# Performance work log

Hardware: AMD Instinct MI355X
Metric: run time of the kernel (lower is better)

Reference implementation:

```python
import jax, jax.numpy as jnp
import numpy as np

EPS = 1e-06


def setup_inputs() -> dict:
    key = jax.random.key(0)
    k1, k2 = jax.random.split(key, 2)
    B, C, T = 8, 256, 8192
    x_real = jax.random.normal(k1, (B, C, T), dtype=jnp.float32)
    x_imag = jax.random.normal(k2, (B, C, T), dtype=jnp.float32)
    # elementwise_affine init: identity * 1/sqrt(2), zero bias
    eye = jnp.eye(2, dtype=jnp.float32)[:, :, None]  # (2,2,1)
    weight = jnp.broadcast_to(eye * 0.70710678118, (2, 2, C)).astype(jnp.float32)
    bias = jnp.zeros((2, C), dtype=jnp.float32)
    return {"x_real": x_real, "x_imag": x_imag, "weight": weight, "bias": bias}


def reference(x_real, x_imag, weight, bias):
    C = x_real.shape[1]
    # (B, C, T, 2) complex-as-last-axis layout
    x = jnp.stack([x_real, x_imag], axis=-1)
    mu = jnp.mean(x, axis=1, keepdims=True)          # per-(b,t) mean over channels
    xc = x - mu                                      # (B, C, T, 2)
    # 2x2 covariance per (b, t), + eps*I for numerical stability
    V = jnp.einsum('bcti,bctj->btij', xc, xc) / C
    V = V + EPS * jnp.eye(2, dtype=x.dtype)
    # Symmetric 2x2 eigendecomposition -> inverse-sqrt whitening matrix
    L, Q = jnp.linalg.eigh(V)                        # L: (B,T,2), Q: (B,T,2,2)
    W = jnp.einsum('btik,btk,btjk->btij', Q, L ** -0.5, Q)  # Q diag(L^-1/2) Q^T
    z = jnp.einsum('bcti,btij->bctj', xc, W)         # whitened (B,C,T,2)
    # per-channel 2x2 affine + bias
    y = jnp.einsum('bcti,ijc->bctj', z, weight) + bias.T[None, :, None, :]
    return y[..., 0], y[..., 1]
```

## Files before the change

### kernel.cpp

```cpp
#include <hip/hip_runtime.h>
#include <math.h>

#define EPS_CLN 1e-6f

constexpr int Bb = 8;
constexpr int Cc = 256;
constexpr int Tt = 8192;

constexpr int TT   = 32;
constexpr int CPT  = 8;
constexpr int NCG  = Cc / CPT;
constexpr int NT4  = TT / 4;
constexpr int NTHR = NCG * NT4;
constexpr int NTB  = Tt / TT;

__global__ __launch_bounds__(NTHR, 4)
void cln_kernel(const float* __restrict__ xr_g, const float* __restrict__ xi_g,
                const float* __restrict__ wgt, const float* __restrict__ bs,
                float* __restrict__ yr_g, float* __restrict__ yi_g) {
    __shared__ float red[5][NCG][TT];
    __shared__ float wlds[5][TT];

    const int tid = threadIdx.x;
    const int t4i = tid & (NT4 - 1);
    const int cg  = tid >> 3;
    const int tb  = blockIdx.x & (NTB - 1);
    const int b   = blockIdx.x >> 8;
    const int tl  = t4i * 4;

    const int cbase = cg * CPT;
    const int base  = (b * Cc + cbase) * Tt + tb * TT + tl;

    float4 xr[CPT], xi[CPT];
#pragma unroll
    for (int k = 0; k < CPT; ++k) {
        xr[k] = *(const float4*)(xr_g + base + k * Tt);
        xi[k] = *(const float4*)(xi_g + base + k * Tt);
    }

    float4 sr = make_float4(0.f, 0.f, 0.f, 0.f);
    float4 si = sr, srr = sr, sri = sr, sii = sr;
#pragma unroll
    for (int k = 0; k < CPT; ++k) {
#define ACC1(c) { float r = xr[k].c, m = xi[k].c;          \
        sr.c += r; si.c += m;                              \
        srr.c = fmaf(r, r, srr.c);                         \
        sri.c = fmaf(r, m, sri.c);                         \
        sii.c = fmaf(m, m, sii.c); }
        ACC1(x) ACC1(y) ACC1(z) ACC1(w)
#undef ACC1
    }

    *(float4*)&red[0][cg][tl] = sr;
    *(float4*)&red[1][cg][tl] = si;
    *(float4*)&red[2][cg][tl] = srr;
    *(float4*)&red[3][cg][tl] = sri;
    *(float4*)&red[4][cg][tl] = sii;
    __syncthreads();

    if (tid < 5 * TT) {
        const int st = tid >> 5;
        const int t  = tid & (TT - 1);
        float s = 0.f;
#pragma unroll
        for (int g = 0; g < NCG; ++g) s += red[st][g][t];
        wlds[st][t] = s;
    }
    __syncthreads();

    if (tid < TT) {
        const float invC = 1.0f / (float)Cc;
        const float mur = wlds[0][tid] * invC, mui = wlds[1][tid] * invC;
        const float a  = fmaf(-mur, mur, wlds[2][tid] * invC) + EPS_CLN;
        const float bb = fmaf(-mur, mui, wlds[3][tid] * invC);
        const float d  = fmaf(-mui, mui, wlds[4][tid] * invC) + EPS_CLN;
        const float s   = sqrtf(fmaf(-bb, bb, a * d));
        const float tau = sqrtf(a + d + 2.0f * s);
        const float inv = 1.0f / (s * tau);
        wlds[0][tid] = mur;
        wlds[1][tid] = mui;
        wlds[2][tid] = (d + s) * inv;
        wlds[3][tid] = -bb * inv;
        wlds[4][tid] = (a + s) * inv;
    }
    __syncthreads();

    const float4 mur = *(const float4*)&wlds[0][tl];
    const float4 mui = *(const float4*)&wlds[1][tl];
    const float4 w00 = *(const float4*)&wlds[2][tl];
    const float4 w01 = *(const float4*)&wlds[3][tl];
    const float4 w11 = *(const float4*)&wlds[4][tl];

#pragma unroll
    for (int k = 0; k < CPT; ++k) {
        const int c = cbase + k;
        const float wt00 = wgt[c];
        const float wt01 = wgt[Cc + c];
        const float wt10 = wgt[2 * Cc + c];
        const float wt11 = wgt[3 * Cc + c];
        const float b0 = bs[c];
        const float b1 = bs[Cc + c];
        float4 yr4, yi4;
#define APP1(cc) {                                         \
        float xcr = xr[k].cc - mur.cc;                     \
        float xci = xi[k].cc - mui.cc;                     \
        float zr = fmaf(xci, w01.cc, xcr * w00.cc);        \
        float zi = fmaf(xcr, w01.cc, xci * w11.cc);        \
        yr4.cc = fmaf(zr, wt00, fmaf(zi, wt10, b0));       \
        yi4.cc = fmaf(zr, wt01, fmaf(zi, wt11, b1)); }
        APP1(x) APP1(y) APP1(z) APP1(w)
#undef APP1
        *(float4*)(yr_g + base + k * Tt) = yr4;
        *(float4*)(yi_g + base + k * Tt) = yi4;
    }
}

extern "C" void kernel_launch(void* const* d_in, const int* in_sizes, int n_in,
                              void* d_out, int out_size, void* d_ws, size_t ws_size,
                              hipStream_t stream) {
    const float* xr  = (const float*)d_in[0];
    const float* xi  = (const float*)d_in[1];
    const float* wgt = (const float*)d_in[2];
    const float* bs  = (const float*)d_in[3];
    float* yr = (float*)d_out;
    float* yi = yr + (size_t)Bb * Cc * Tt;
    dim3 grid(Bb * NTB);
    cln_kernel<<<grid, NTHR, 0, stream>>>(xr, xi, wgt, bs, yr, yi);
}
```

Before: 45.58 us.

## Replace LDS block reduction with per-wavefront shuffle reduction over channels

Each wavefront now owns 16 time steps across all 256 channels, with each lane holding 16 channels. The channel statistics are reduced with xor shuffles inside the wavefront, and every lane computes the whitening matrix redundantly. This removes the shared-memory reduction, the three block barriers and the serialized single-thread whitening step. In exchange each thread holds twice as many registers, and each row access is only 64 bytes wide, which may hurt memory coalescing and occupancy.

```diff
diff --git a/kernel.cpp b/kernel.cpp
--- a/kernel.cpp
+++ b/kernel.cpp
@@ -7,41 +7,38 @@
 constexpr int Cc = 256;
 constexpr int Tt = 8192;
 
-constexpr int TT   = 32;
-constexpr int CPT  = 8;
-constexpr int NCG  = Cc / CPT;
-constexpr int NT4  = TT / 4;
-constexpr int NTHR = NCG * NT4;
-constexpr int NTB  = Tt / TT;
+constexpr int TTW  = 16;
+constexpr int CPTL = 16;
+constexpr int WPB  = 4;
+constexpr int NTHR = 64 * WPB;
+constexpr int CHNK = Tt / TTW;
+constexpr int NBLK = Bb * CHNK / WPB;
 
-__global__ __launch_bounds__(NTHR, 4)
+__global__ __launch_bounds__(NTHR, 1)
 void cln_kernel(const float* __restrict__ xr_g, const float* __restrict__ xi_g,
                 const float* __restrict__ wgt, const float* __restrict__ bs,
                 float* __restrict__ yr_g, float* __restrict__ yi_g) {
-    __shared__ float red[5][NCG][TT];
-    __shared__ float wlds[5][TT];
+    const int tid  = threadIdx.x;
+    const int lane = tid & 63;
+    const int gw   = blockIdx.x * WPB + (tid >> 6);
+    const int b    = gw >> 9;
+    const int t0   = (gw & (CHNK - 1)) * TTW;
+    const int cg   = lane >> 2;
+    const int t4   = lane & 3;
+    const int cbase = cg * CPTL;
+    const size_t base = (size_t)(b * Cc + cbase) * Tt + t0 + t4 * 4;
 
-    const int tid = threadIdx.x;
-    const int t4i = tid & (NT4 - 1);
-    const int cg  = tid >> 3;
-    const int tb  = blockIdx.x & (NTB - 1);
-    const int b   = blockIdx.x >> 8;
-    const int tl  = t4i * 4;
-
-    const int cbase = cg * CPT;
-    const int base  = (b * Cc + cbase) * Tt + tb * TT + tl;
-
-    float4 xr[CPT], xi[CPT];
+    float4 xr[CPTL], xi[CPTL];
 #pragma unroll
-    for (int k = 0; k < CPT; ++k) {
-        xr[k] = *(const float4*)(xr_g + base + k * Tt);
-        xi[k] = *(const float4*)(xi_g + base + k * Tt);
+    for (int k = 0; k < CPTL; ++k) {
+        xr[k] = *(const float4*)(xr_g + base + (size_t)k * Tt);
+        xi[k] = *(const float4*)(xi_g + base + (size_t)k * Tt);
     }
 
     float4 sr = make_float4(0.f, 0.f, 0.f, 0.f);
     float4 si = sr, srr = sr, sri = sr, sii = sr;
 #pragma unroll
-    for (int k = 0; k < CPT; ++k) {
+    for (int k = 0; k < CPTL; ++k) {
 #define ACC1(c) { float r = xr[k].c, m = xi[k].c;          \
         sr.c += r; si.c += m;                              \
         srr.c = fmaf(r, r, srr.c);                         \
@@ -51,48 +48,31 @@
 #undef ACC1
     }
 
-    *(float4*)&red[0][cg][tl] = sr;
-    *(float4*)&red[1][cg][tl] = si;
-    *(float4*)&red[2][cg][tl] = srr;
-    *(float4*)&red[3][cg][tl] = sri;
-    *(float4*)&red[4][cg][tl] = sii;
-    __syncthreads();
+#define REDC(v, cc, mask) v.cc += __shfl_xor(v.cc, mask);
+#define REDV(v, mask) REDC(v,x,mask) REDC(v,y,mask) REDC(v,z,mask) REDC(v,w,mask)
+#define REDALL(mask) REDV(sr,mask) REDV(si,mask) REDV(srr,mask) REDV(sri,mask) REDV(sii,mask)
+    REDALL(4) REDALL(8) REDALL(16) REDALL(32)
+#undef REDALL
+#undef REDV
+#undef REDC
 
-    if (tid < 5 * TT) {
-        const int st = tid >> 5;
-        const int t  = tid & (TT - 1);
-        float s = 0.f;
-#pragma unroll
-        for (int g = 0; g < NCG; ++g) s += red[st][g][t];
-        wlds[st][t] = s;
-    }
-    __syncthreads();
-
-    if (tid < TT) {
-        const float invC = 1.0f / (float)Cc;
-        const float mur = wlds[0][tid] * invC, mui = wlds[1][tid] * invC;
-        const float a  = fmaf(-mur, mur, wlds[2][tid] * invC) + EPS_CLN;
-        const float bb = fmaf(-mur, mui, wlds[3][tid] * invC);
-        const float d  = fmaf(-mui, mui, wlds[4][tid] * invC) + EPS_CLN;
-        const float s   = sqrtf(fmaf(-bb, bb, a * d));
-        const float tau = sqrtf(a + d + 2.0f * s);
-        const float inv = 1.0f / (s * tau);
-        wlds[0][tid] = mur;
-        wlds[1][tid] = mui;
-        wlds[2][tid] = (d + s) * inv;
-        wlds[3][tid] = -bb * inv;
-        wlds[4][tid] = (a + s) * inv;
-    }
-    __syncthreads();
-
-    const float4 mur = *(const float4*)&wlds[0][tl];
-    const float4 mui = *(const float4*)&wlds[1][tl];
-    const float4 w00 = *(const float4*)&wlds[2][tl];
-    const float4 w01 = *(const float4*)&wlds[3][tl];
-    const float4 w11 = *(const float4*)&wlds[4][tl];
+    const float invC = 1.0f / (float)Cc;
+    float4 mur, mui, w00, w01, w11;
+#define WCOMP(cc) {                                                 \
+    float mr = sr.cc * invC, mi = si.cc * invC;                     \
+    float a  = fmaf(-mr, mr, srr.cc * invC) + EPS_CLN;              \
+    float bv = fmaf(-mr, mi, sri.cc * invC);                        \
+    float d  = fmaf(-mi, mi, sii.cc * invC) + EPS_CLN;              \
+    float s   = sqrtf(fmaf(-bv, bv, a * d));                        \
+    float tau = sqrtf(a + d + 2.0f * s);                            \
+    float inv = 1.0f / (s * tau);                                   \
+    mur.cc = mr; mui.cc = mi;                                       \
+    w00.cc = (d + s) * inv; w01.cc = -bv * inv; w11.cc = (a + s) * inv; }
+    WCOMP(x) WCOMP(y) WCOMP(z) WCOMP(w)
+#undef WCOMP
 
 #pragma unroll
-    for (int k = 0; k < CPT; ++k) {
+    for (int k = 0; k < CPTL; ++k) {
         const int c = cbase + k;
         const float wt00 = wgt[c];
         const float wt01 = wgt[Cc + c];
@@ -110,8 +90,8 @@
         yi4.cc = fmaf(zr, wt01, fmaf(zi, wt11, b1)); }
         APP1(x) APP1(y) APP1(z) APP1(w)
 #undef APP1
-        *(float4*)(yr_g + base + k * Tt) = yr4;
-        *(float4*)(yi_g + base + k * Tt) = yi4;
+        *(float4*)(yr_g + base + (size_t)k * Tt) = yr4;
+        *(float4*)(yi_g + base + (size_t)k * Tt) = yi4;
     }
 }
 
@@ -124,6 +104,5 @@
     const float* bs  = (const float*)d_in[3];
     float* yr = (float*)d_out;
     float* yi = yr + (size_t)Bb * Cc * Tt;
-    dim3 grid(Bb * NTB);
-    cln_kernel<<<grid, NTHR, 0, stream>>>(xr, xi, wgt, bs, yr, yi);
+    cln_kernel<<<dim3(NBLK), NTHR, 0, stream>>>(xr, xi, wgt, bs, yr, yi);
 }
```

Result: slower. 50.02 us (+9.7%).
